# Optimization experiments

Hardware: AMD Instinct MI355X
Metric: run time of the kernel (lower is better)

The kernel has to match this reference:

```python
import jax, jax.numpy as jnp
import numpy as np

N_NODES = 50000
N_EDGES = 800000
N_GRAPHS = 2000
F = 256          # node feature dim == hidden_dim (required by stacked convs)
HID = 256
L = 4
FP = 1034
BN_EPS = 1e-5


def setup_inputs() -> dict:
    key = jax.random.key(0)
    ks = jax.random.split(key, 20)
    s = 0.05
    x = jax.random.normal(ks[0], (N_NODES, F), dtype=jnp.float32)
    edge_index = jax.random.randint(ks[1], (2, N_EDGES), 0, N_NODES, dtype=jnp.int64)
    edge_attr = jax.random.normal(ks[2], (N_EDGES, 1), dtype=jnp.float32)
    fingerprint = jax.random.uniform(ks[3], (N_GRAPHS, FP), dtype=jnp.float32)
    batch = jnp.sort(jax.random.randint(ks[4], (N_NODES,), 0, N_GRAPHS, dtype=jnp.int64))
    # stacked per-layer conv params: message linear [(F+1)->HID], update linear [HID->HID]
    lin_w = jax.random.normal(ks[5], (L, F + 1, HID), dtype=jnp.float32) * s
    lin_b = jax.random.normal(ks[6], (L, HID), dtype=jnp.float32) * s
    upd_w = jax.random.normal(ks[7], (L, HID, HID), dtype=jnp.float32) * s
    upd_b = jax.random.normal(ks[8], (L, HID), dtype=jnp.float32) * s
    # gated-attention pooling gate_nn: Linear(HID,HID) -> tanh -> Linear(HID,1)
    g1_w = jax.random.normal(ks[9], (HID, HID), dtype=jnp.float32) * s
    g1_b = jax.random.normal(ks[10], (HID,), dtype=jnp.float32) * s
    g2_w = jax.random.normal(ks[11], (HID, 1), dtype=jnp.float32) * s
    g2_b = jax.random.normal(ks[12], (1,), dtype=jnp.float32) * s
    fc1_w = jax.random.normal(ks[13], (HID + FP, HID), dtype=jnp.float32) * s
    fc1_b = jax.random.normal(ks[14], (HID,), dtype=jnp.float32) * s
    bn_gamma = jnp.ones((HID,), dtype=jnp.float32)
    bn_beta = jnp.zeros((HID,), dtype=jnp.float32)
    fc2_w = jax.random.normal(ks[15], (HID, 1), dtype=jnp.float32) * s
    fc2_b = jax.random.normal(ks[16], (1,), dtype=jnp.float32) * s
    return dict(x=x, edge_index=edge_index, edge_attr=edge_attr,
                fingerprint=fingerprint, batch=batch,
                lin_w=lin_w, lin_b=lin_b, upd_w=upd_w, upd_b=upd_b,
                g1_w=g1_w, g1_b=g1_b, g2_w=g2_w, g2_b=g2_b,
                fc1_w=fc1_w, fc1_b=fc1_b, bn_gamma=bn_gamma, bn_beta=bn_beta,
                fc2_w=fc2_w, fc2_b=fc2_b)


def reference(x, edge_index, edge_attr, fingerprint, batch,
              lin_w, lin_b, upd_w, upd_b,
              g1_w, g1_b, g2_w, g2_b,
              fc1_w, fc1_b, bn_gamma, bn_beta, fc2_w, fc2_b):
    n = x.shape[0]
    b = fingerprint.shape[0]
    loop = jnp.arange(n, dtype=edge_index.dtype)
    src = jnp.concatenate([edge_index[0], loop])   # x_j = source nodes (PyG default)
    dst = jnp.concatenate([edge_index[1], loop])   # aggregate at target
    ea = jnp.concatenate([edge_attr, jnp.zeros((n, edge_attr.shape[1]), edge_attr.dtype)], axis=0)
    for l in range(L):
        wn, we = lin_w[l, :F], lin_w[l, F:]        # split concat([x_j, edge_attr]) @ W
        msg = jax.nn.relu(x[src] @ wn + ea @ we + lin_b[l])          # [E+n, HID]
        aggr = jax.ops.segment_sum(msg, dst, num_segments=n)          # scatter-add
        x = jax.nn.relu(aggr @ upd_w[l] + upd_b[l])
    # gated attention pooling
    gate = jax.nn.sigmoid(jnp.tanh(x @ g1_w + g1_b) @ g2_w + g2_b)    # [n, 1]
    pooled = jax.ops.segment_sum(x * gate, batch, num_segments=b)     # [b, HID]
    h = jnp.concatenate([pooled, fingerprint], axis=1) @ fc1_w + fc1_b
    # BatchNorm1d (training mode: biased batch stats)
    mu = jnp.mean(h, axis=0)
    var = jnp.mean((h - mu) ** 2, axis=0)
    h = (h - mu) * jax.lax.rsqrt(var + BN_EPS) * bn_gamma + bn_beta
    h = jax.nn.relu(h)  # dropout is identity in eval mode
    return (h @ fc2_w + fc2_b).squeeze(-1)        # [b]
```

## Files before the change

kernel.cpp:

```cpp
#include <hip/hip_runtime.h>
#include <math.h>

#define HIDF 256
#define FPDIM 1034
#define MPAD 50048
#define FCM 2048
#define FCK 1344

typedef _Float16 f16x8 __attribute__((ext_vector_type(8)));
typedef _Float16 f16x4 __attribute__((ext_vector_type(4)));
typedef float f32x4 __attribute__((ext_vector_type(4)));

__device__ __forceinline__ float relu_f(float v) { return fmaxf(v, 0.f); }

__global__ __launch_bounds__(256) void convxh_k(
    const float* __restrict__ x, _Float16* __restrict__ xh, int n)
{
    int i = blockIdx.x * 256 + threadIdx.x;
    int row = i >> 6;
    if (row >= MPAD) return;
    f16x4 o;
    if (row < n) {
        float4 v = ((const float4*)x)[i];
        o[0] = (_Float16)v.x; o[1] = (_Float16)v.y;
        o[2] = (_Float16)v.z; o[3] = (_Float16)v.w;
    } else {
        o[0] = o[1] = o[2] = o[3] = (_Float16)0.f;
    }
    ((f16x4*)xh)[i] = o;
}

__global__ __launch_bounds__(256) void convw_k(
    const float* __restrict__ w, _Float16* __restrict__ whi,
    _Float16* __restrict__ wlo)
{
    int i = blockIdx.x * 256 + threadIdx.x;
    int nn = i >> 8, kk = i & 255;
    float v = w[kk * 256 + nn];
    _Float16 h = (_Float16)v;
    _Float16 l = (_Float16)(v - (float)h);
    whi[i] = h;
    wlo[i] = l;
}

__global__ __launch_bounds__(256) void convfc1a_k(
    const float* __restrict__ pooled, const float* __restrict__ fp,
    _Float16* __restrict__ ahi, _Float16* __restrict__ alo, int B)
{
    int i = blockIdx.x * 256 + threadIdx.x;
    if (i >= FCM * FCK) return;
    int row = i / FCK, col = i - row * FCK;
    float v = 0.f;
    if (row < B) {
        if (col < HIDF) v = pooled[(size_t)row * HIDF + col];
        else if (col < HIDF + FPDIM) v = fp[(size_t)row * FPDIM + (col - HIDF)];
    }
    _Float16 h = (_Float16)v;
    _Float16 l = (_Float16)(v - (float)h);
    ahi[i] = h;
    alo[i] = l;
}

__global__ __launch_bounds__(256) void convfc1w_k(
    const float* __restrict__ w, _Float16* __restrict__ whi,
    _Float16* __restrict__ wlo)
{
    int i = blockIdx.x * 256 + threadIdx.x;
    if (i >= HIDF * FCK) return;
    int nn = i / FCK, kk = i - nn * FCK;
    float v = (kk < HIDF + FPDIM) ? w[(size_t)kk * HIDF + nn] : 0.f;
    _Float16 h = (_Float16)v;
    _Float16 l = (_Float16)(v - (float)h);
    whi[i] = h;
    wlo[i] = l;
}

template <int ACT>
__global__ __launch_bounds__(256) void gemm_f16(
    const _Float16* __restrict__ A, const _Float16* __restrict__ Whi,
    const _Float16* __restrict__ Wlo, const float* __restrict__ bias,
    _Float16* __restrict__ C, int M, int N, int K)
{
    __shared__ _Float16 As[128 * 64];
    __shared__ _Float16 Bh[128 * 64];
    __shared__ _Float16 Bl[128 * 64];
    const int tid = threadIdx.x;
    const int wave = tid >> 6, lane = tid & 63;
    const int m0 = blockIdx.y * 128, n0 = blockIdx.x * 128;
    const int wr = wave >> 1, wc = wave & 1;

    f32x4 acc[4][4];
#pragma unroll
    for (int i = 0; i < 4; ++i)
#pragma unroll
        for (int j = 0; j < 4; ++j) acc[i][j] = (f32x4){0.f, 0.f, 0.f, 0.f};

    const int lrow = lane >> 3;
    const int lcol8 = (lane & 7) * 8;

    for (int k0 = 0; k0 < K; k0 += 64) {
#pragma unroll
        for (int i = 0; i < 4; ++i) {
            int iss = wave * 4 + i;
            int row = 8 * iss + lrow;
            const _Float16* ga = A   + (size_t)(m0 + row) * K + k0 + lcol8;
            const _Float16* gh = Whi + (size_t)(n0 + row) * K + k0 + lcol8;
            const _Float16* gl = Wlo + (size_t)(n0 + row) * K + k0 + lcol8;
            __builtin_amdgcn_global_load_lds(
                (const __attribute__((address_space(1))) void*)ga,
                (__attribute__((address_space(3))) void*)(As + iss * 512), 16, 0, 0);
            __builtin_amdgcn_global_load_lds(
                (const __attribute__((address_space(1))) void*)gh,
                (__attribute__((address_space(3))) void*)(Bh + iss * 512), 16, 0, 0);
            __builtin_amdgcn_global_load_lds(
                (const __attribute__((address_space(1))) void*)gl,
                (__attribute__((address_space(3))) void*)(Bl + iss * 512), 16, 0, 0);
        }
        __syncthreads();
#pragma unroll
        for (int kk = 0; kk < 2; ++kk) {
            const int kb = kk * 32 + (lane >> 4) * 8;
            f16x8 af[4], bh[4], bl[4];
#pragma unroll
            for (int mi = 0; mi < 4; ++mi)
                af[mi] = *(const f16x8*)&As[(wr * 64 + mi * 16 + (lane & 15)) * 64 + kb];
#pragma unroll
            for (int ni = 0; ni < 4; ++ni) {
                int r = (wc * 64 + ni * 16 + (lane & 15)) * 64 + kb;
                bh[ni] = *(const f16x8*)&Bh[r];
                bl[ni] = *(const f16x8*)&Bl[r];
            }
#pragma unroll
            for (int mi = 0; mi < 4; ++mi)
#pragma unroll
                for (int ni = 0; ni < 4; ++ni) {
                    acc[mi][ni] = __builtin_amdgcn_mfma_f32_16x16x32_f16(
                        af[mi], bh[ni], acc[mi][ni], 0, 0, 0);
                    acc[mi][ni] = __builtin_amdgcn_mfma_f32_16x16x32_f16(
                        af[mi], bl[ni], acc[mi][ni], 0, 0, 0);
                }
        }
        __syncthreads();
    }

    const int crow0 = m0 + wr * 64 + (lane >> 4) * 4;
    const int ccol0 = n0 + wc * 64 + (lane & 15);
#pragma unroll
    for (int mi = 0; mi < 4; ++mi) {
#pragma unroll
        for (int ni = 0; ni < 4; ++ni) {
            int col = ccol0 + ni * 16;
            float bv = bias ? bias[col] : 0.f;
#pragma unroll
            for (int r = 0; r < 4; ++r) {
                int row = crow0 + mi * 16 + r;
                float v = acc[mi][ni][r] + bv;
                if (ACT == 1) v = relu_f(v);
                else if (ACT == 2) v = tanhf(v);
                C[(size_t)row * N + col] = (_Float16)v;
            }
        }
    }
}

__global__ __launch_bounds__(256) void gemm_fc1(
    const _Float16* __restrict__ Ahi, const _Float16* __restrict__ Alo,
    const _Float16* __restrict__ Whi, const _Float16* __restrict__ Wlo,
    const float* __restrict__ bias, float* __restrict__ C,
    int Mv, int N, int K)
{
    __shared__ _Float16 Ah[128 * 64];
    __shared__ _Float16 Al[128 * 64];
    __shared__ _Float16 Bh[128 * 64];
    __shared__ _Float16 Bl[128 * 64];
    const int tid = threadIdx.x;
    const int wave = tid >> 6, lane = tid & 63;
    const int m0 = blockIdx.y * 128, n0 = blockIdx.x * 128;
    const int wr = wave >> 1, wc = wave & 1;

    f32x4 acc[4][4];
#pragma unroll
    for (int i = 0; i < 4; ++i)
#pragma unroll
        for (int j = 0; j < 4; ++j) acc[i][j] = (f32x4){0.f, 0.f, 0.f, 0.f};

    const int lrow = lane >> 3;
    const int lcol8 = (lane & 7) * 8;

    for (int k0 = 0; k0 < K; k0 += 64) {
#pragma unroll
        for (int i = 0; i < 4; ++i) {
            int iss = wave * 4 + i;
            int row = 8 * iss + lrow;
            const _Float16* gah = Ahi + (size_t)(m0 + row) * K + k0 + lcol8;
            const _Float16* gal = Alo + (size_t)(m0 + row) * K + k0 + lcol8;
            const _Float16* gbh = Whi + (size_t)(n0 + row) * K + k0 + lcol8;
            const _Float16* gbl = Wlo + (size_t)(n0 + row) * K + k0 + lcol8;
            __builtin_amdgcn_global_load_lds(
                (const __attribute__((address_space(1))) void*)gah,
                (__attribute__((address_space(3))) void*)(Ah + iss * 512), 16, 0, 0);
            __builtin_amdgcn_global_load_lds(
                (const __attribute__((address_space(1))) void*)gal,
                (__attribute__((address_space(3))) void*)(Al + iss * 512), 16, 0, 0);
            __builtin_amdgcn_global_load_lds(
                (const __attribute__((address_space(1))) void*)gbh,
                (__attribute__((address_space(3))) void*)(Bh + iss * 512), 16, 0, 0);
            __builtin_amdgcn_global_load_lds(
                (const __attribute__((address_space(1))) void*)gbl,
                (__attribute__((address_space(3))) void*)(Bl + iss * 512), 16, 0, 0);
        }
        __syncthreads();
#pragma unroll
        for (int kk = 0; kk < 2; ++kk) {
            const int kb = kk * 32 + (lane >> 4) * 8;
            f16x8 ah[4], al[4], bh[4], bl[4];
#pragma unroll
            for (int mi = 0; mi < 4; ++mi) {
                int r = (wr * 64 + mi * 16 + (lane & 15)) * 64 + kb;
                ah[mi] = *(const f16x8*)&Ah[r];
                al[mi] = *(const f16x8*)&Al[r];
            }
#pragma unroll
            for (int ni = 0; ni < 4; ++ni) {
                int r = (wc * 64 + ni * 16 + (lane & 15)) * 64 + kb;
                bh[ni] = *(const f16x8*)&Bh[r];
                bl[ni] = *(const f16x8*)&Bl[r];
            }
#pragma unroll
            for (int mi = 0; mi < 4; ++mi)
#pragma unroll
                for (int ni = 0; ni < 4; ++ni) {
                    acc[mi][ni] = __builtin_amdgcn_mfma_f32_16x16x32_f16(
                        ah[mi], bh[ni], acc[mi][ni], 0, 0, 0);
                    acc[mi][ni] = __builtin_amdgcn_mfma_f32_16x16x32_f16(
                        ah[mi], bl[ni], acc[mi][ni], 0, 0, 0);
                    acc[mi][ni] = __builtin_amdgcn_mfma_f32_16x16x32_f16(
                        al[mi], bh[ni], acc[mi][ni], 0, 0, 0);
                }
        }
        __syncthreads();
    }

    const int crow0 = m0 + wr * 64 + (lane >> 4) * 4;
    const int ccol0 = n0 + wc * 64 + (lane & 15);
#pragma unroll
    for (int mi = 0; mi < 4; ++mi) {
#pragma unroll
        for (int ni = 0; ni < 4; ++ni) {
            int col = ccol0 + ni * 16;
            float bv = bias[col];
#pragma unroll
            for (int r = 0; r < 4; ++r) {
                int row = crow0 + mi * 16 + r;
                if (row < Mv)
                    C[(size_t)row * N + col] = acc[mi][ni][r] + bv;
            }
        }
    }
}

__global__ void count_k(const int* __restrict__ dst, int* __restrict__ cnt, int E)
{
    int e = blockIdx.x * blockDim.x + threadIdx.x;
    if (e < E) atomicAdd(&cnt[dst[e]], 1);
}

__global__ __launch_bounds__(256) void scan1_k(
    const int* __restrict__ cnt, int* __restrict__ offs,
    int* __restrict__ bsum, int n)
{
    __shared__ int sh[256];
    int t = threadIdx.x, idx = blockIdx.x * 256 + t;
    int v = (idx < n) ? cnt[idx] : 0;
    sh[t] = v;
    __syncthreads();
    for (int o = 1; o < 256; o <<= 1) {
        int a = (t >= o) ? sh[t - o] : 0;
        __syncthreads();
        sh[t] += a;
        __syncthreads();
    }
    if (idx < n) offs[idx] = sh[t] - v;
    if (t == 255) bsum[blockIdx.x] = sh[255];
}

__global__ __launch_bounds__(256) void scan2_k(int* __restrict__ bsum, int nb)
{
    __shared__ int sh[256];
    int t = threadIdx.x;
    int v = (t < nb) ? bsum[t] : 0;
    sh[t] = v;
    __syncthreads();
    for (int o = 1; o < 256; o <<= 1) {
        int a = (t >= o) ? sh[t - o] : 0;
        __syncthreads();
        sh[t] += a;
        __syncthreads();
    }
    if (t < nb) bsum[t] = sh[t] - v;
}

__global__ __launch_bounds__(256) void scan3_k(
    int* __restrict__ offs, const int* __restrict__ bsum,
    int* __restrict__ cursor, int n, int E)
{
    int idx = blockIdx.x * 256 + threadIdx.x;
    if (idx < n) {
        int o = offs[idx] + bsum[blockIdx.x];
        offs[idx] = o;
        cursor[idx] = o;
    }
    if (idx == 0) offs[n] = E;
}

__global__ void scatter_k(const int* __restrict__ dst, const int* __restrict__ src,
                          const float* __restrict__ ea, int* __restrict__ cursor,
                          int2* __restrict__ esrc, int E)
{
    int e = blockIdx.x * blockDim.x + threadIdx.x;
    if (e < E) {
        int p = atomicAdd(&cursor[dst[e]], 1);
        esrc[p] = make_int2(src[e], __float_as_int(ea[e]));
    }
}

__global__ void start_k(const int* __restrict__ batch, int* __restrict__ start,
                        int n, int B)
{
    int g = blockIdx.x * blockDim.x + threadIdx.x;
    if (g > B) return;
    int lo = 0, hi = n;
    while (lo < hi) {
        int mid = (lo + hi) >> 1;
        if (batch[mid] < g) lo = mid + 1; else hi = mid;
    }
    start[g] = lo;
}

__global__ __launch_bounds__(256) void aggregate_k(
    const _Float16* __restrict__ xw, const float* __restrict__ we,
    const int2* __restrict__ esrc, const int* __restrict__ offs,
    _Float16* __restrict__ out, int n)
{
    int w = (blockIdx.x * blockDim.x + threadIdx.x) >> 6;
    if (w >= n) return;
    const int lane = threadIdx.x & 63;
    const int half = lane >> 5;
    const int f8 = (lane & 31) << 3;

    float we8[8];
    *(float4*)&we8[0] = *(const float4*)(we + f8);
    *(float4*)&we8[4] = *(const float4*)(we + f8 + 4);

    f16x8 xs = *(const f16x8*)(xw + (size_t)w * HIDF + f8);
    float acc[8];
#pragma unroll
    for (int j = 0; j < 8; ++j)
        acc[j] = (half == 0) ? relu_f((float)xs[j]) : 0.f;

    const int e0 = offs[w], e1 = offs[w + 1];
    const int cntE = e1 - e0;
    const int fullPairs = cntE >> 1;

    int t = 0;
    for (; t + 4 <= fullPairs; t += 4) {
        int2 p[4]; f16x8 v[4];
#pragma unroll
        for (int q = 0; q < 4; ++q) p[q] = esrc[e0 + 2 * (t + q) + half];
#pragma unroll
        for (int q = 0; q < 4; ++q)
            v[q] = *(const f16x8*)(xw + (size_t)p[q].x * HIDF + f8);
#pragma unroll
        for (int q = 0; q < 4; ++q) {
            float a = __int_as_float(p[q].y);
#pragma unroll
            for (int j = 0; j < 8; ++j)
                acc[j] += relu_f(fmaf(a, we8[j], (float)v[q][j]));
        }
    }
    for (; t < fullPairs; ++t) {
        int2 p = esrc[e0 + 2 * t + half];
        f16x8 v = *(const f16x8*)(xw + (size_t)p.x * HIDF + f8);
        float a = __int_as_float(p.y);
#pragma unroll
        for (int j = 0; j < 8; ++j)
            acc[j] += relu_f(fmaf(a, we8[j], (float)v[j]));
    }
    if ((cntE & 1) && half == 0) {
        int2 p = esrc[e1 - 1];
        f16x8 v = *(const f16x8*)(xw + (size_t)p.x * HIDF + f8);
        float a = __int_as_float(p.y);
#pragma unroll
        for (int j = 0; j < 8; ++j)
            acc[j] += relu_f(fmaf(a, we8[j], (float)v[j]));
    }

#pragma unroll
    for (int j = 0; j < 8; ++j)
        acc[j] += __shfl_xor(acc[j], 32);

    if (half == 0) {
        f16x8 o;
#pragma unroll
        for (int j = 0; j < 8; ++j) o[j] = (_Float16)acc[j];
        *(f16x8*)(out + (size_t)w * HIDF + f8) = o;
    }
}

__global__ __launch_bounds__(256) void gate_k(
    const _Float16* __restrict__ t, const float* __restrict__ g2w,
    const float* __restrict__ g2b, float* __restrict__ gate, int n)
{
    int w = (blockIdx.x * blockDim.x + threadIdx.x) >> 6;
    if (w >= n) return;
    int lane = threadIdx.x & 63;
    f16x4 tv = *(const f16x4*)(t + (size_t)w * HIDF + (lane << 2));
    float4 g = *(const float4*)(g2w + (lane << 2));
    float s = (float)tv[0] * g.x + (float)tv[1] * g.y
            + (float)tv[2] * g.z + (float)tv[3] * g.w;
    for (int o = 32; o; o >>= 1) s += __shfl_xor(s, o);
    if (lane == 0) gate[w] = 1.f / (1.f + expf(-(s + g2b[0])));
}

__global__ __launch_bounds__(256) void pool_k(
    const _Float16* __restrict__ x, const float* __restrict__ gate,
    const int* __restrict__ start, float* __restrict__ pooled, int B)
{
    int w = (blockIdx.x * blockDim.x + threadIdx.x) >> 6;
    if (w >= B) return;
    int lane = threadIdx.x & 63;
    int f = lane << 2;
    float4 acc = make_float4(0.f, 0.f, 0.f, 0.f);
    int i0 = start[w], i1 = start[w + 1];
    for (int i = i0; i < i1; ++i) {
        float gi = gate[i];
        f16x4 v = *(const f16x4*)(x + (size_t)i * HIDF + f);
        acc.x = fmaf(gi, (float)v[0], acc.x);
        acc.y = fmaf(gi, (float)v[1], acc.y);
        acc.z = fmaf(gi, (float)v[2], acc.z);
        acc.w = fmaf(gi, (float)v[3], acc.w);
    }
    *(float4*)(pooled + (size_t)w * HIDF + f) = acc;
}

__global__ __launch_bounds__(256) void bnstats_k(
    const float* __restrict__ h, float* __restrict__ mu,
    float* __restrict__ rs, int B)
{
    int j = blockIdx.x;
    int tid = threadIdx.x;
    float s = 0.f, s2 = 0.f;
    for (int g = tid; g < B; g += 256) {
        float v = h[(size_t)g * HIDF + j];
        s += v;
        s2 = fmaf(v, v, s2);
    }
    __shared__ float sh[256], sh2[256];
    sh[tid] = s; sh2[tid] = s2;
    __syncthreads();
    for (int o = 128; o; o >>= 1) {
        if (tid < o) { sh[tid] += sh[tid + o]; sh2[tid] += sh2[tid + o]; }
        __syncthreads();
    }
    if (tid == 0) {
        float m = sh[0] / (float)B;
        float var = sh2[0] / (float)B - m * m;
        if (var < 0.f) var = 0.f;
        mu[j] = m;
        rs[j] = rsqrtf(var + 1e-5f);
    }
}

__global__ __launch_bounds__(256) void final_k(
    const float* __restrict__ h, const float* __restrict__ mu,
    const float* __restrict__ rs, const float* __restrict__ gamma,
    const float* __restrict__ beta, const float* __restrict__ w2,
    const float* __restrict__ b2, float* __restrict__ out, int B)
{
    int g = blockIdx.x;
    int j = threadIdx.x;
    float v = h[(size_t)g * HIDF + j];
    v = (v - mu[j]) * rs[j] * gamma[j] + beta[j];
    v = relu_f(v);
    float term = v * w2[j];
    __shared__ float sh[256];
    sh[j] = term;
    __syncthreads();
    for (int o = 128; o; o >>= 1) {
        if (j < o) sh[j] += sh[j + o];
        __syncthreads();
    }
    if (j == 0) out[g] = sh[0] + b2[0];
}

extern "C" void kernel_launch(void* const* d_in, const int* in_sizes, int n_in,
                              void* d_out, int out_size, void* d_ws, size_t ws_size,
                              hipStream_t stream)
{
    const float* x      = (const float*)d_in[0];
    const int*   ei     = (const int*)d_in[1];
    const float* ea     = (const float*)d_in[2];
    const float* fp     = (const float*)d_in[3];
    const int*   batch  = (const int*)d_in[4];
    const float* lin_w  = (const float*)d_in[5];
    const float* lin_b  = (const float*)d_in[6];
    const float* upd_w  = (const float*)d_in[7];
    const float* upd_b  = (const float*)d_in[8];
    const float* g1w    = (const float*)d_in[9];
    const float* g1b    = (const float*)d_in[10];
    const float* g2w    = (const float*)d_in[11];
    const float* g2b    = (const float*)d_in[12];
    const float* fc1w   = (const float*)d_in[13];
    const float* fc1b   = (const float*)d_in[14];
    const float* gamma  = (const float*)d_in[15];
    const float* beta   = (const float*)d_in[16];
    const float* fc2w   = (const float*)d_in[17];
    const float* fc2b   = (const float*)d_in[18];
    float* out = (float*)d_out;

    const int n = in_sizes[0] / HIDF;
    const int E = in_sizes[1] / 2;
    const int B = in_sizes[3] / FPDIM;
    const int L = in_sizes[5] / (257 * 256);
    const int* srcArr = ei;
    const int* dstArr = ei + E;
    const int nb = (n + 255) / 256;

    char* w = (char*)d_ws;
    _Float16* xh   = (_Float16*)w;  w += (size_t)MPAD * HIDF * 2;
    _Float16* bufA = (_Float16*)w;  w += (size_t)MPAD * HIDF * 2;
    _Float16* bufB = (_Float16*)w;  w += (size_t)MPAD * HIDF * 2;
    _Float16* whi = (_Float16*)w;  w += (size_t)9 * 65536 * 2;
    _Float16* wlo = (_Float16*)w;  w += (size_t)9 * 65536 * 2;
    _Float16* fahi = (_Float16*)w; w += (size_t)FCM * FCK * 2;
    _Float16* falo = (_Float16*)w; w += (size_t)FCM * FCK * 2;
    _Float16* fwhi = (_Float16*)w; w += (size_t)HIDF * FCK * 2;
    _Float16* fwlo = (_Float16*)w; w += (size_t)HIDF * FCK * 2;
    int2*  esrc   = (int2*)w;   w += (size_t)E * 8;
    int*   offs   = (int*)w;    w += ((size_t)n + 4) * 4;
    int*   cursor = (int*)w;    w += ((size_t)n + 4) * 4;
    int*   cnt    = (int*)w;    w += (size_t)n * 4;
    int*   bsum   = (int*)w;    w += 256 * 4;
    int*   startA = (int*)w;    w += ((size_t)B + 4) * 4;
    float* gateA  = (float*)w;  w += (size_t)n * 4;
    float* pooled = (float*)w;  w += (size_t)B * HIDF * 4;
    float* h      = (float*)w;  w += (size_t)B * HIDF * 4;
    float* mu     = (float*)w;  w += 256 * 4;
    float* rs     = (float*)w;  w += 256 * 4;

    hipMemsetAsync(cnt, 0, (size_t)n * 4, stream);
    count_k<<<(E + 255) / 256, 256, 0, stream>>>(dstArr, cnt, E);
    scan1_k<<<nb, 256, 0, stream>>>(cnt, offs, bsum, n);
    scan2_k<<<1, 256, 0, stream>>>(bsum, nb);
    scan3_k<<<nb, 256, 0, stream>>>(offs, bsum, cursor, n, E);
    scatter_k<<<(E + 255) / 256, 256, 0, stream>>>(dstArr, srcArr, ea, cursor, esrc, E);
    start_k<<<(B + 256) / 256, 256, 0, stream>>>(batch, startA, n, B);

    convxh_k<<<(MPAD * 64 + 255) / 256, 256, 0, stream>>>(x, xh, n);
    for (int l = 0; l < L; ++l) {
        convw_k<<<256, 256, 0, stream>>>(lin_w + (size_t)l * 257 * 256,
                                         whi + (size_t)l * 65536, wlo + (size_t)l * 65536);
        convw_k<<<256, 256, 0, stream>>>(upd_w + (size_t)l * 65536,
                                         whi + (size_t)(4 + l) * 65536, wlo + (size_t)(4 + l) * 65536);
    }
    convw_k<<<256, 256, 0, stream>>>(g1w, whi + (size_t)8 * 65536, wlo + (size_t)8 * 65536);
    convfc1w_k<<<(HIDF * FCK + 255) / 256, 256, 0, stream>>>(fc1w, fwhi, fwlo);

    dim3 ggm(HIDF / 128, MPAD / 128);
    for (int l = 0; l < L; ++l) {
        const float* we = lin_w + (size_t)l * 257 * 256 + 256 * 256;
        const float* lb = lin_b + (size_t)l * 256;
        gemm_f16<0><<<ggm, 256, 0, stream>>>(xh, whi + (size_t)l * 65536,
                                             wlo + (size_t)l * 65536, lb,
                                             bufA, MPAD, HIDF, HIDF);
        aggregate_k<<<(n * 64 + 255) / 256, 256, 0, stream>>>(
            bufA, we, esrc, offs, bufB, n);
        gemm_f16<1><<<ggm, 256, 0, stream>>>(bufB, whi + (size_t)(4 + l) * 65536,
                                             wlo + (size_t)(4 + l) * 65536,
                                             upd_b + (size_t)l * 256, xh, MPAD, HIDF, HIDF);
    }

    gemm_f16<2><<<ggm, 256, 0, stream>>>(xh, whi + (size_t)8 * 65536,
                                         wlo + (size_t)8 * 65536, g1b,
                                         bufA, MPAD, HIDF, HIDF);
    gate_k<<<(n * 64 + 255) / 256, 256, 0, stream>>>(bufA, g2w, g2b, gateA, n);
    pool_k<<<(B * 64 + 255) / 256, 256, 0, stream>>>(xh, gateA, startA, pooled, B);

    convfc1a_k<<<(FCM * FCK + 255) / 256, 256, 0, stream>>>(pooled, fp, fahi, falo, B);
    dim3 ggf(HIDF / 128, FCM / 128);
    gemm_fc1<<<ggf, 256, 0, stream>>>(fahi, falo, fwhi, fwlo, fc1b, h, B, HIDF, FCK);
    bnstats_k<<<256, 256, 0, stream>>>(h, mu, rs, B);
    final_k<<<B, 256, 0, stream>>>(h, mu, rs, gamma, beta, fc2w, fc2b, out, B);
}
```

Measured before the change: 714.0 us.

## Widen node GEMM tiles, split-K fc1 with atomics, merge weight conversions

The node GEMMs now use 512-thread blocks that each cover all 256 output columns, so every A tile is loaded once instead of twice. The fc1 GEMM is split into three K slices that accumulate into a zeroed output with atomicAdd, which adds parallelism for this small-M problem; the bias add moves into the BN kernels. The nine weight-conversion launches are merged into one 2D launch, and the aggregation unroll goes from 4 to 8 edges. The risks are higher LDS and register use per block in the node GEMM, and nondeterministic float summation order in fc1.

```diff
diff --git a/kernel.cpp b/kernel.cpp
--- a/kernel.cpp
+++ b/kernel.cpp
@@ -6,6 +6,8 @@
 #define MPAD 50048
 #define FCM 2048
 #define FCK 1344
+#define FCSLICES 3
+#define FCKSLICE 448
 
 typedef _Float16 f16x8 __attribute__((ext_vector_type(8)));
 typedef _Float16 f16x4 __attribute__((ext_vector_type(4)));
@@ -30,17 +32,22 @@
     ((f16x4*)xh)[i] = o;
 }
 
-__global__ __launch_bounds__(256) void convw_k(
-    const float* __restrict__ w, _Float16* __restrict__ whi,
+__global__ __launch_bounds__(256) void convw_all_k(
+    const float* __restrict__ lin_w, const float* __restrict__ upd_w,
+    const float* __restrict__ g1w, _Float16* __restrict__ whi,
     _Float16* __restrict__ wlo)
 {
+    int m = blockIdx.y;
+    const float* src = (m < 4) ? (lin_w + (size_t)m * 257 * 256)
+                     : (m < 8) ? (upd_w + (size_t)(m - 4) * 65536)
+                               : g1w;
     int i = blockIdx.x * 256 + threadIdx.x;
     int nn = i >> 8, kk = i & 255;
-    float v = w[kk * 256 + nn];
+    float v = src[kk * 256 + nn];
     _Float16 h = (_Float16)v;
     _Float16 l = (_Float16)(v - (float)h);
-    whi[i] = h;
-    wlo[i] = l;
+    whi[(size_t)m * 65536 + i] = h;
+    wlo[(size_t)m * 65536 + i] = l;
 }
 
 __global__ __launch_bounds__(256) void convfc1a_k(
@@ -76,18 +83,19 @@
 }
 
 template <int ACT>
-__global__ __launch_bounds__(256) void gemm_f16(
+__global__ __launch_bounds__(512) void gemm_f16(
     const _Float16* __restrict__ A, const _Float16* __restrict__ Whi,
     const _Float16* __restrict__ Wlo, const float* __restrict__ bias,
-    _Float16* __restrict__ C, int M, int N, int K)
-{
+    _Float16* __restrict__ C, int M)
+{
+    const int N = 256, K = 256;
     __shared__ _Float16 As[128 * 64];
-    __shared__ _Float16 Bh[128 * 64];
-    __shared__ _Float16 Bl[128 * 64];
+    __shared__ _Float16 Bh[256 * 64];
+    __shared__ _Float16 Bl[256 * 64];
     const int tid = threadIdx.x;
-    const int wave = tid >> 6, lane = tid & 63;
-    const int m0 = blockIdx.y * 128, n0 = blockIdx.x * 128;
-    const int wr = wave >> 1, wc = wave & 1;
+    const int wid = tid >> 6, lane = tid & 63;
+    const int m0 = blockIdx.y * 128;
+    const int wr = wid >> 2, wc = wid & 3;
 
     f32x4 acc[4][4];
 #pragma unroll
@@ -100,15 +108,20 @@
 
     for (int k0 = 0; k0 < K; k0 += 64) {
 #pragma unroll
-        for (int i = 0; i < 4; ++i) {
-            int iss = wave * 4 + i;
+        for (int i = 0; i < 2; ++i) {
+            int iss = wid * 2 + i;
             int row = 8 * iss + lrow;
-            const _Float16* ga = A   + (size_t)(m0 + row) * K + k0 + lcol8;
-            const _Float16* gh = Whi + (size_t)(n0 + row) * K + k0 + lcol8;
-            const _Float16* gl = Wlo + (size_t)(n0 + row) * K + k0 + lcol8;
+            const _Float16* ga = A + (size_t)(m0 + row) * K + k0 + lcol8;
             __builtin_amdgcn_global_load_lds(
                 (const __attribute__((address_space(1))) void*)ga,
                 (__attribute__((address_space(3))) void*)(As + iss * 512), 16, 0, 0);
+        }
+#pragma unroll
+        for (int i = 0; i < 4; ++i) {
+            int iss = wid * 4 + i;
+            int row = 8 * iss + lrow;
+            const _Float16* gh = Whi + (size_t)row * K + k0 + lcol8;
+            const _Float16* gl = Wlo + (size_t)row * K + k0 + lcol8;
             __builtin_amdgcn_global_load_lds(
                 (const __attribute__((address_space(1))) void*)gh,
                 (__attribute__((address_space(3))) void*)(Bh + iss * 512), 16, 0, 0);
@@ -144,7 +157,7 @@
     }
 
     const int crow0 = m0 + wr * 64 + (lane >> 4) * 4;
-    const int ccol0 = n0 + wc * 64 + (lane & 15);
+    const int ccol0 = wc * 64 + (lane & 15);
 #pragma unroll
     for (int mi = 0; mi < 4; ++mi) {
 #pragma unroll
@@ -166,8 +179,7 @@
 __global__ __launch_bounds__(256) void gemm_fc1(
     const _Float16* __restrict__ Ahi, const _Float16* __restrict__ Alo,
     const _Float16* __restrict__ Whi, const _Float16* __restrict__ Wlo,
-    const float* __restrict__ bias, float* __restrict__ C,
-    int Mv, int N, int K)
+    float* __restrict__ C, int Mv, int N, int K)
 {
     __shared__ _Float16 Ah[128 * 64];
     __shared__ _Float16 Al[128 * 64];
@@ -176,6 +188,8 @@
     const int tid = threadIdx.x;
     const int wave = tid >> 6, lane = tid & 63;
     const int m0 = blockIdx.y * 128, n0 = blockIdx.x * 128;
+    const int kbeg = blockIdx.z * FCKSLICE;
+    const int kend = kbeg + FCKSLICE;
     const int wr = wave >> 1, wc = wave & 1;
 
     f32x4 acc[4][4];
@@ -187,7 +201,7 @@
     const int lrow = lane >> 3;
     const int lcol8 = (lane & 7) * 8;
 
-    for (int k0 = 0; k0 < K; k0 += 64) {
+    for (int k0 = kbeg; k0 < kend; k0 += 64) {
 #pragma unroll
         for (int i = 0; i < 4; ++i) {
             int iss = wave * 4 + i;
@@ -248,12 +262,11 @@
 #pragma unroll
         for (int ni = 0; ni < 4; ++ni) {
             int col = ccol0 + ni * 16;
-            float bv = bias[col];
 #pragma unroll
             for (int r = 0; r < 4; ++r) {
                 int row = crow0 + mi * 16 + r;
                 if (row < Mv)
-                    C[(size_t)row * N + col] = acc[mi][ni][r] + bv;
+                    atomicAdd(&C[(size_t)row * N + col], acc[mi][ni][r]);
             }
         }
     }
@@ -363,15 +376,15 @@
     const int fullPairs = cntE >> 1;
 
     int t = 0;
-    for (; t + 4 <= fullPairs; t += 4) {
-        int2 p[4]; f16x8 v[4];
-#pragma unroll
-        for (int q = 0; q < 4; ++q) p[q] = esrc[e0 + 2 * (t + q) + half];
-#pragma unroll
-        for (int q = 0; q < 4; ++q)
+    for (; t + 8 <= fullPairs; t += 8) {
+        int2 p[8]; f16x8 v[8];
+#pragma unroll
+        for (int q = 0; q < 8; ++q) p[q] = esrc[e0 + 2 * (t + q) + half];
+#pragma unroll
+        for (int q = 0; q < 8; ++q)
             v[q] = *(const f16x8*)(xw + (size_t)p[q].x * HIDF + f8);
 #pragma unroll
-        for (int q = 0; q < 4; ++q) {
+        for (int q = 0; q < 8; ++q) {
             float a = __int_as_float(p[q].y);
 #pragma unroll
             for (int j = 0; j < 8; ++j)
@@ -444,14 +457,15 @@
 }
 
 __global__ __launch_bounds__(256) void bnstats_k(
-    const float* __restrict__ h, float* __restrict__ mu,
-    float* __restrict__ rs, int B)
+    const float* __restrict__ h, const float* __restrict__ fc1b,
+    float* __restrict__ mu, float* __restrict__ rs, int B)
 {
     int j = blockIdx.x;
     int tid = threadIdx.x;
+    float bj = fc1b[j];
     float s = 0.f, s2 = 0.f;
     for (int g = tid; g < B; g += 256) {
-        float v = h[(size_t)g * HIDF + j];
+        float v = h[(size_t)g * HIDF + j] + bj;
         s += v;
         s2 = fmaf(v, v, s2);
     }
@@ -472,14 +486,15 @@
 }
 
 __global__ __launch_bounds__(256) void final_k(
-    const float* __restrict__ h, const float* __restrict__ mu,
-    const float* __restrict__ rs, const float* __restrict__ gamma,
-    const float* __restrict__ beta, const float* __restrict__ w2,
-    const float* __restrict__ b2, float* __restrict__ out, int B)
+    const float* __restrict__ h, const float* __restrict__ fc1b,
+    const float* __restrict__ mu, const float* __restrict__ rs,
+    const float* __restrict__ gamma, const float* __restrict__ beta,
+    const float* __restrict__ w2, const float* __restrict__ b2,
+    float* __restrict__ out, int B)
 {
     int g = blockIdx.x;
     int j = threadIdx.x;
-    float v = h[(size_t)g * HIDF + j];
+    float v = h[(size_t)g * HIDF + j] + fc1b[j];
     v = (v - mu[j]) * rs[j] * gamma[j] + beta[j];
     v = relu_f(v);
     float term = v * w2[j];
@@ -557,38 +572,32 @@
     start_k<<<(B + 256) / 256, 256, 0, stream>>>(batch, startA, n, B);
 
     convxh_k<<<(MPAD * 64 + 255) / 256, 256, 0, stream>>>(x, xh, n);
-    for (int l = 0; l < L; ++l) {
-        convw_k<<<256, 256, 0, stream>>>(lin_w + (size_t)l * 257 * 256,
-                                         whi + (size_t)l * 65536, wlo + (size_t)l * 65536);
-        convw_k<<<256, 256, 0, stream>>>(upd_w + (size_t)l * 65536,
-                                         whi + (size_t)(4 + l) * 65536, wlo + (size_t)(4 + l) * 65536);
-    }
-    convw_k<<<256, 256, 0, stream>>>(g1w, whi + (size_t)8 * 65536, wlo + (size_t)8 * 65536);
+    dim3 gcw(256, 9);
+    convw_all_k<<<gcw, 256, 0, stream>>>(lin_w, upd_w, g1w, whi, wlo);
     convfc1w_k<<<(HIDF * FCK + 255) / 256, 256, 0, stream>>>(fc1w, fwhi, fwlo);
 
-    dim3 ggm(HIDF / 128, MPAD / 128);
+    dim3 ggm(1, MPAD / 128);
     for (int l = 0; l < L; ++l) {
         const float* we = lin_w + (size_t)l * 257 * 256 + 256 * 256;
         const float* lb = lin_b + (size_t)l * 256;
-        gemm_f16<0><<<ggm, 256, 0, stream>>>(xh, whi + (size_t)l * 65536,
-                                             wlo + (size_t)l * 65536, lb,
-                                             bufA, MPAD, HIDF, HIDF);
+        gemm_f16<0><<<ggm, 512, 0, stream>>>(xh, whi + (size_t)l * 65536,
+                                             wlo + (size_t)l * 65536, lb, bufA, MPAD);
         aggregate_k<<<(n * 64 + 255) / 256, 256, 0, stream>>>(
             bufA, we, esrc, offs, bufB, n);
-        gemm_f16<1><<<ggm, 256, 0, stream>>>(bufB, whi + (size_t)(4 + l) * 65536,
+        gemm_f16<1><<<ggm, 512, 0, stream>>>(bufB, whi + (size_t)(4 + l) * 65536,
                                              wlo + (size_t)(4 + l) * 65536,
-                                             upd_b + (size_t)l * 256, xh, MPAD, HIDF, HIDF);
-    }
-
-    gemm_f16<2><<<ggm, 256, 0, stream>>>(xh, whi + (size_t)8 * 65536,
-                                         wlo + (size_t)8 * 65536, g1b,
-                                         bufA, MPAD, HIDF, HIDF);
+                                             upd_b + (size_t)l * 256, xh, MPAD);
+    }
+
+    gemm_f16<2><<<ggm, 512, 0, stream>>>(xh, whi + (size_t)8 * 65536,
+                                         wlo + (size_t)8 * 65536, g1b, bufA, MPAD);
     gate_k<<<(n * 64 + 255) / 256, 256, 0, stream>>>(bufA, g2w, g2b, gateA, n);
     pool_k<<<(B * 64 + 255) / 256, 256, 0, stream>>>(xh, gateA, startA, pooled, B);
 
     convfc1a_k<<<(FCM * FCK + 255) / 256, 256, 0, stream>>>(pooled, fp, fahi, falo, B);
-    dim3 ggf(HIDF / 128, FCM / 128);
-    gemm_fc1<<<ggf, 256, 0, stream>>>(fahi, falo, fwhi, fwlo, fc1b, h, B, HIDF, FCK);
-    bnstats_k<<<256, 256, 0, stream>>>(h, mu, rs, B);
-    final_k<<<B, 256, 0, stream>>>(h, mu, rs, gamma, beta, fc2w, fc2b, out, B);
-}
+    hipMemsetAsync(h, 0, (size_t)B * HIDF * 4, stream);
+    dim3 ggf(HIDF / 128, FCM / 128, FCSLICES);
+    gemm_fc1<<<ggf, 256, 0, stream>>>(fahi, falo, fwhi, fwlo, h, B, HIDF, FCK);
+    bnstats_k<<<256, 256, 0, stream>>>(h, fc1b, mu, rs, B);
+    final_k<<<B, 256, 0, stream>>>(h, fc1b, mu, rs, gamma, beta, fc2w, fc2b, out, B);
+}
```

Measured after the change: 788.5 us. +10.4%, slower.
